# Performance work log

Measured on AMD Instinct MI355X. Metric: run time of the kernel, lower is better.

The kernel has to match this reference:

```python
import jax, jax.numpy as jnp
import numpy as np

N, C, H, K = 100000, 64, 8, 16
D = C // H  # head_dim = 8


def setup_inputs() -> dict:
    key = jax.random.key(0)
    ks = jax.random.split(key, 7)
    s = 1.0 / np.sqrt(C)
    return {
        "feats": jax.random.normal(ks[0], (N, C), jnp.float32),
        "knn_idx": jax.random.randint(ks[1], (N, K), 0, N, jnp.int32),
        "Wq": jax.random.normal(ks[2], (C, C), jnp.float32) * s,
        "Wk": jax.random.normal(ks[3], (C, C), jnp.float32) * s,
        "Wv": jax.random.normal(ks[4], (C, C), jnp.float32) * s,
        "Wo": jax.random.normal(ks[5], (C, C), jnp.float32) * s,
        "bo": jnp.zeros((C,), jnp.float32),
    }


def reference(feats, knn_idx, Wq, Wk, Wv, Wo, bo):
    # Projections (torch Linear y = x @ W^T expressed with pre-transposed W)
    q = (feats @ Wq).reshape(N, H, D)          # [N,H,D]
    k_feat = (feats @ Wk).reshape(N, H, D)     # [N,H,D]
    v = (feats @ Wv).reshape(N, H, D)          # [N,H,D]

    # Gather k-NN neighbors: [N,K,H,D]
    k_nb = k_feat[knn_idx]
    v_nb = v[knn_idx]

    # Scores: dot(q, k_neighbor) per head, scaled
    scores = jnp.einsum("nhd,nkhd->nkh", q, k_nb) / np.sqrt(D).astype(np.float32)
    attn = jax.nn.softmax(scores, axis=1)      # softmax over K neighbors

    out = jnp.einsum("nkh,nkhd->nhd", attn, v_nb).reshape(N, C)
    return out @ Wo + bo
```

## Files before the change

kernel.cpp:

```cpp
#include <hip/hip_runtime.h>
#include <hip/hip_fp16.h>
#include <math.h>

#define NPTS 100000
#define CDIM 64
#define KNN  16

typedef unsigned int uint;
typedef _Float16 f16x8 __attribute__((ext_vector_type(8)));
typedef float    f32x4 __attribute__((ext_vector_type(4)));

template <int CTRL>
__device__ __forceinline__ float dpp_add(float x) {
    int yi = __builtin_amdgcn_mov_dpp(__float_as_int(x), CTRL, 0xF, 0xF, true);
    return x + __int_as_float(yi);
}

__device__ __forceinline__ f16x8 load_bfrag(const float* W, int ks, int quad,
                                            int ct, int m) {
    const float* wp = W + (size_t)(ks * 32 + quad * 8) * 64 + ct * 16 + m;
    f16x8 b;
    #pragma unroll
    for (int j = 0; j < 8; ++j) b[j] = (_Float16)wp[j * 64];
    return b;
}

__device__ __forceinline__ f16x8 load_afrag(const float* fp, int ks, int quad) {
    const float4 x0 = *(const float4*)(fp + ks * 32 + quad * 8);
    const float4 x1 = *(const float4*)(fp + ks * 32 + quad * 8 + 4);
    f16x8 a;
    a[0] = (_Float16)x0.x; a[1] = (_Float16)x0.y;
    a[2] = (_Float16)x0.z; a[3] = (_Float16)x0.w;
    a[4] = (_Float16)x1.x; a[5] = (_Float16)x1.y;
    a[6] = (_Float16)x1.z; a[7] = (_Float16)x1.w;
    return a;
}

__global__ __launch_bounds__(256) void proj_qkv(
    const float* __restrict__ feats,
    const float* __restrict__ Wq, const float* __restrict__ Wk,
    const float* __restrict__ Wv,
    float* __restrict__ q, uint* __restrict__ kv)
{
    const int lane = threadIdx.x & 63;
    const int m = lane & 15, quad = lane >> 4;

    f16x8 Bf[3][4][2];
    #pragma unroll
    for (int ct = 0; ct < 4; ++ct)
        #pragma unroll
        for (int ks = 0; ks < 2; ++ks) {
            Bf[0][ct][ks] = load_bfrag(Wq, ks, quad, ct, m);
            Bf[1][ct][ks] = load_bfrag(Wk, ks, quad, ct, m);
            Bf[2][ct][ks] = load_bfrag(Wv, ks, quad, ct, m);
        }

    const int wid = blockIdx.x * 4 + (threadIdx.x >> 6);
    const int nw = gridDim.x * 4;
    for (int tile = wid; tile < NPTS / 16; tile += nw) {
        const int r0 = tile * 16;
        const float* fp = feats + (size_t)(r0 + m) * 64;
        f16x8 Af0 = load_afrag(fp, 0, quad);
        f16x8 Af1 = load_afrag(fp, 1, quad);

        #pragma unroll
        for (int ct = 0; ct < 4; ++ct) {
            f32x4 aq = {0.f, 0.f, 0.f, 0.f};
            f32x4 ak = {0.f, 0.f, 0.f, 0.f};
            f32x4 av = {0.f, 0.f, 0.f, 0.f};
            aq = __builtin_amdgcn_mfma_f32_16x16x32_f16(Af0, Bf[0][ct][0], aq, 0, 0, 0);
            aq = __builtin_amdgcn_mfma_f32_16x16x32_f16(Af1, Bf[0][ct][1], aq, 0, 0, 0);
            ak = __builtin_amdgcn_mfma_f32_16x16x32_f16(Af0, Bf[1][ct][0], ak, 0, 0, 0);
            ak = __builtin_amdgcn_mfma_f32_16x16x32_f16(Af1, Bf[1][ct][1], ak, 0, 0, 0);
            av = __builtin_amdgcn_mfma_f32_16x16x32_f16(Af0, Bf[2][ct][0], av, 0, 0, 0);
            av = __builtin_amdgcn_mfma_f32_16x16x32_f16(Af1, Bf[2][ct][1], av, 0, 0, 0);

            const int col = ct * 16 + m;
            #pragma unroll
            for (int r = 0; r < 4; ++r) {
                const size_t off = (size_t)(r0 + quad * 4 + r) * 64 + col;
                q[off] = aq[r];
                kv[off] = (uint)__half_as_ushort(__float2half(ak[r]))
                        | ((uint)__half_as_ushort(__float2half(av[r])) << 16);
            }
        }
    }
}

__global__ __launch_bounds__(256) void attn_mid(
    const float* __restrict__ q, const uint* __restrict__ kv,
    const int* __restrict__ knn, float* __restrict__ o_mid)
{
    const int t = threadIdx.x;
    const int lane = t & 63;
    const int n = blockIdx.x * 4 + (t >> 6);
    const int ns = __builtin_amdgcn_readfirstlane(n);

    const float qv = q[(size_t)n * 64 + lane];

    const int* kr = knn + (size_t)ns * KNN;
    int idx[KNN];
    #pragma unroll
    for (int i = 0; i < KNN; ++i) idx[i] = kr[i];

    float sc[KNN], vr[KNN];
    #pragma unroll
    for (int i = 0; i < KNN; ++i) {
        const uint w = kv[(size_t)idx[i] * 64 + lane];
        const float2 kvf = __half22float2(*(const __half2*)&w);
        vr[i] = kvf.y;
        float p = qv * kvf.x;
        p = dpp_add<0xB1>(p);
        p = dpp_add<0x4E>(p);
        p = dpp_add<0x141>(p);
        sc[i] = p * 0.3535533905932738f;
    }

    float m = sc[0];
    #pragma unroll
    for (int i = 1; i < KNN; ++i) m = fmaxf(m, sc[i]);
    float s = 0.f;
    #pragma unroll
    for (int i = 0; i < KNN; ++i) { sc[i] = __expf(sc[i] - m); s += sc[i]; }
    const float inv = 1.f / s;

    float acc = 0.f;
    #pragma unroll
    for (int i = 0; i < KNN; ++i) acc += sc[i] * vr[i];

    o_mid[(size_t)n * 64 + lane] = acc * inv;
}

__global__ __launch_bounds__(256) void out_proj(
    const float* __restrict__ o_mid, const float* __restrict__ Wo,
    const float* __restrict__ bo, float* __restrict__ out)
{
    const int lane = threadIdx.x & 63;
    const int m = lane & 15, quad = lane >> 4;

    f16x8 Bf[4][2];
    float bias[4];
    #pragma unroll
    for (int ct = 0; ct < 4; ++ct) {
        bias[ct] = bo[ct * 16 + m];
        #pragma unroll
        for (int ks = 0; ks < 2; ++ks)
            Bf[ct][ks] = load_bfrag(Wo, ks, quad, ct, m);
    }

    const int wid = blockIdx.x * 4 + (threadIdx.x >> 6);
    const int nw = gridDim.x * 4;
    for (int tile = wid; tile < NPTS / 16; tile += nw) {
        const int r0 = tile * 16;
        const float* fp = o_mid + (size_t)(r0 + m) * 64;
        f16x8 Af0 = load_afrag(fp, 0, quad);
        f16x8 Af1 = load_afrag(fp, 1, quad);

        #pragma unroll
        for (int ct = 0; ct < 4; ++ct) {
            f32x4 ac = {0.f, 0.f, 0.f, 0.f};
            ac = __builtin_amdgcn_mfma_f32_16x16x32_f16(Af0, Bf[ct][0], ac, 0, 0, 0);
            ac = __builtin_amdgcn_mfma_f32_16x16x32_f16(Af1, Bf[ct][1], ac, 0, 0, 0);

            const int col = ct * 16 + m;
            #pragma unroll
            for (int r = 0; r < 4; ++r)
                out[(size_t)(r0 + quad * 4 + r) * 64 + col] = ac[r] + bias[ct];
        }
    }
}

extern "C" void kernel_launch(void* const* d_in, const int* in_sizes, int n_in,
                              void* d_out, int out_size, void* d_ws, size_t ws_size,
                              hipStream_t stream) {
    const float* feats = (const float*)d_in[0];
    const int*   knn   = (const int*)d_in[1];
    const float* Wq    = (const float*)d_in[2];
    const float* Wk    = (const float*)d_in[3];
    const float* Wv    = (const float*)d_in[4];
    const float* Wo    = (const float*)d_in[5];
    const float* bo    = (const float*)d_in[6];
    float* out = (float*)d_out;

    float* q     = (float*)d_ws;
    uint*  kvbuf = (uint*)(q + (size_t)NPTS * CDIM);
    float* o_mid = (float*)(kvbuf + (size_t)NPTS * CDIM);

    proj_qkv<<<512, 256, 0, stream>>>(feats, Wq, Wk, Wv, q, kvbuf);
    attn_mid<<<NPTS / 4, 256, 0, stream>>>(q, kvbuf, knn, o_mid);
    out_proj<<<512, 256, 0, stream>>>(o_mid, Wo, bo, out);
}
```

Before: 169.3 us.

## Fuse attention with output projection, prepack weight fragments, store q in fp16

Adds a one-block kernel that packs all four weight matrices into fp16 MFMA fragment layout once, so the projection kernels load fragments with a single vector load instead of strided scalar gathers. The attention kernel now handles 16 points per block, stages the attention output in shared memory and applies the output projection with MFMA in place, which removes the o_mid round trip through global memory and one launch. q is stored as fp16, halving its traffic at a small precision cost, and proj_qkv switches to one tile per wave with many more blocks. This adds an extra tiny launch and a block barrier in the attention kernel.

```diff
diff --git a/kernel.cpp b/kernel.cpp
--- a/kernel.cpp
+++ b/kernel.cpp
@@ -16,13 +16,27 @@
     return x + __int_as_float(yi);
 }
 
-__device__ __forceinline__ f16x8 load_bfrag(const float* W, int ks, int quad,
-                                            int ct, int m) {
-    const float* wp = W + (size_t)(ks * 32 + quad * 8) * 64 + ct * 16 + m;
-    f16x8 b;
-    #pragma unroll
-    for (int j = 0; j < 8; ++j) b[j] = (_Float16)wp[j * 64];
-    return b;
+
+__global__ __launch_bounds__(256) void pack_w(
+    const float* __restrict__ Wq, const float* __restrict__ Wk,
+    const float* __restrict__ Wv, const float* __restrict__ Wo,
+    __half* __restrict__ frag)
+{
+    const float* Ws[4] = {Wq, Wk, Wv, Wo};
+    f16x8* fp = (f16x8*)frag;
+    for (int e = threadIdx.x; e < 2048; e += 256) {
+        const int lane = e & 63;
+        const int ks   = (e >> 6) & 1;
+        const int ct   = (e >> 7) & 3;
+        const int mat  = e >> 9;
+        const int m = lane & 15, quad = lane >> 4;
+        const float* W = Ws[mat];
+        f16x8 b;
+        #pragma unroll
+        for (int j = 0; j < 8; ++j)
+            b[j] = (_Float16)W[(size_t)(ks * 32 + quad * 8 + j) * 64 + ct * 16 + m];
+        fp[e] = b;
+    }
 }
 
 __device__ __forceinline__ f16x8 load_afrag(const float* fp, int ks, int quad) {
@@ -37,137 +51,136 @@
 }
 
 __global__ __launch_bounds__(256) void proj_qkv(
-    const float* __restrict__ feats,
-    const float* __restrict__ Wq, const float* __restrict__ Wk,
-    const float* __restrict__ Wv,
-    float* __restrict__ q, uint* __restrict__ kv)
+    const float* __restrict__ feats, const __half* __restrict__ frag,
+    __half* __restrict__ q, uint* __restrict__ kv)
 {
+    const int wid = blockIdx.x * 4 + (threadIdx.x >> 6);
+    if (wid >= NPTS / 16) return;
     const int lane = threadIdx.x & 63;
     const int m = lane & 15, quad = lane >> 4;
 
+    const f16x8* fp = (const f16x8*)frag;
     f16x8 Bf[3][4][2];
     #pragma unroll
-    for (int ct = 0; ct < 4; ++ct)
-        #pragma unroll
-        for (int ks = 0; ks < 2; ++ks) {
-            Bf[0][ct][ks] = load_bfrag(Wq, ks, quad, ct, m);
-            Bf[1][ct][ks] = load_bfrag(Wk, ks, quad, ct, m);
-            Bf[2][ct][ks] = load_bfrag(Wv, ks, quad, ct, m);
+    for (int mat = 0; mat < 3; ++mat)
+        #pragma unroll
+        for (int ct = 0; ct < 4; ++ct)
+            #pragma unroll
+            for (int ks = 0; ks < 2; ++ks)
+                Bf[mat][ct][ks] = fp[((mat * 4 + ct) * 2 + ks) * 64 + lane];
+
+    const int r0 = wid * 16;
+    const float* ap = feats + (size_t)(r0 + m) * 64;
+    const f16x8 Af0 = load_afrag(ap, 0, quad);
+    const f16x8 Af1 = load_afrag(ap, 1, quad);
+
+    #pragma unroll
+    for (int ct = 0; ct < 4; ++ct) {
+        f32x4 aq = {0.f, 0.f, 0.f, 0.f};
+        f32x4 ak = {0.f, 0.f, 0.f, 0.f};
+        f32x4 av = {0.f, 0.f, 0.f, 0.f};
+        aq = __builtin_amdgcn_mfma_f32_16x16x32_f16(Af0, Bf[0][ct][0], aq, 0, 0, 0);
+        aq = __builtin_amdgcn_mfma_f32_16x16x32_f16(Af1, Bf[0][ct][1], aq, 0, 0, 0);
+        ak = __builtin_amdgcn_mfma_f32_16x16x32_f16(Af0, Bf[1][ct][0], ak, 0, 0, 0);
+        ak = __builtin_amdgcn_mfma_f32_16x16x32_f16(Af1, Bf[1][ct][1], ak, 0, 0, 0);
+        av = __builtin_amdgcn_mfma_f32_16x16x32_f16(Af0, Bf[2][ct][0], av, 0, 0, 0);
+        av = __builtin_amdgcn_mfma_f32_16x16x32_f16(Af1, Bf[2][ct][1], av, 0, 0, 0);
+
+        const int col = ct * 16 + m;
+        #pragma unroll
+        for (int r = 0; r < 4; ++r) {
+            const size_t off = (size_t)(r0 + quad * 4 + r) * 64 + col;
+            q[off] = __float2half(aq[r]);
+            kv[off] = (uint)__half_as_ushort(__float2half(ak[r]))
+                    | ((uint)__half_as_ushort(__float2half(av[r])) << 16);
         }
-
-    const int wid = blockIdx.x * 4 + (threadIdx.x >> 6);
-    const int nw = gridDim.x * 4;
-    for (int tile = wid; tile < NPTS / 16; tile += nw) {
-        const int r0 = tile * 16;
-        const float* fp = feats + (size_t)(r0 + m) * 64;
-        f16x8 Af0 = load_afrag(fp, 0, quad);
-        f16x8 Af1 = load_afrag(fp, 1, quad);
-
-        #pragma unroll
-        for (int ct = 0; ct < 4; ++ct) {
-            f32x4 aq = {0.f, 0.f, 0.f, 0.f};
-            f32x4 ak = {0.f, 0.f, 0.f, 0.f};
-            f32x4 av = {0.f, 0.f, 0.f, 0.f};
-            aq = __builtin_amdgcn_mfma_f32_16x16x32_f16(Af0, Bf[0][ct][0], aq, 0, 0, 0);
-            aq = __builtin_amdgcn_mfma_f32_16x16x32_f16(Af1, Bf[0][ct][1], aq, 0, 0, 0);
-            ak = __builtin_amdgcn_mfma_f32_16x16x32_f16(Af0, Bf[1][ct][0], ak, 0, 0, 0);
-            ak = __builtin_amdgcn_mfma_f32_16x16x32_f16(Af1, Bf[1][ct][1], ak, 0, 0, 0);
-            av = __builtin_amdgcn_mfma_f32_16x16x32_f16(Af0, Bf[2][ct][0], av, 0, 0, 0);
-            av = __builtin_amdgcn_mfma_f32_16x16x32_f16(Af1, Bf[2][ct][1], av, 0, 0, 0);
-
-            const int col = ct * 16 + m;
-            #pragma unroll
-            for (int r = 0; r < 4; ++r) {
-                const size_t off = (size_t)(r0 + quad * 4 + r) * 64 + col;
-                q[off] = aq[r];
-                kv[off] = (uint)__half_as_ushort(__float2half(ak[r]))
-                        | ((uint)__half_as_ushort(__float2half(av[r])) << 16);
-            }
-        }
-    }
-}
-
-__global__ __launch_bounds__(256) void attn_mid(
-    const float* __restrict__ q, const uint* __restrict__ kv,
-    const int* __restrict__ knn, float* __restrict__ o_mid)
+    }
+}
+
+__global__ __launch_bounds__(256) void attn_out(
+    const __half* __restrict__ q, const uint* __restrict__ kv,
+    const int* __restrict__ knn, const __half* __restrict__ frag,
+    const float* __restrict__ bo, float* __restrict__ out)
 {
+    __shared__ float sO[16][68];
     const int t = threadIdx.x;
     const int lane = t & 63;
-    const int n = blockIdx.x * 4 + (t >> 6);
-    const int ns = __builtin_amdgcn_readfirstlane(n);
-
-    const float qv = q[(size_t)n * 64 + lane];
-
-    const int* kr = knn + (size_t)ns * KNN;
-    int idx[KNN];
+    const int w = t >> 6;
+    const int m = lane & 15, quad = lane >> 4;
+
+    const f16x8* fpb = (const f16x8*)frag;
+    const f16x8 Wf0 = fpb[((3 * 4 + w) * 2 + 0) * 64 + lane];
+    const f16x8 Wf1 = fpb[((3 * 4 + w) * 2 + 1) * 64 + lane];
+    const float bias = bo[w * 16 + m];
+
+    const int n0 = blockIdx.x * 16;
+
+    #pragma unroll 1
+    for (int p = 0; p < 4; ++p) {
+        const int n = n0 + w * 4 + p;
+        const int ns = __builtin_amdgcn_readfirstlane(n);
+
+        const float qv = __half2float(q[(size_t)n * 64 + lane]);
+
+        const int* kr = knn + (size_t)ns * KNN;
+        int idx[KNN];
+        #pragma unroll
+        for (int i = 0; i < KNN; ++i) idx[i] = kr[i];
+
+        float sc[KNN], vr[KNN];
+        #pragma unroll
+        for (int i = 0; i < KNN; ++i) {
+            const uint wv = kv[(size_t)idx[i] * 64 + lane];
+            const float2 kvf = __half22float2(*(const __half2*)&wv);
+            vr[i] = kvf.y;
+            float pr = qv * kvf.x;
+            pr = dpp_add<0xB1>(pr);
+            pr = dpp_add<0x4E>(pr);
+            pr = dpp_add<0x141>(pr);
+            sc[i] = pr * 0.3535533905932738f;
+        }
+
+        float mx = sc[0];
+        #pragma unroll
+        for (int i = 1; i < KNN; ++i) mx = fmaxf(mx, sc[i]);
+        float s = 0.f;
+        #pragma unroll
+        for (int i = 0; i < KNN; ++i) { sc[i] = __expf(sc[i] - mx); s += sc[i]; }
+        const float inv = 1.f / s;
+
+        float acc = 0.f;
+        #pragma unroll
+        for (int i = 0; i < KNN; ++i) acc += sc[i] * vr[i];
+
+        sO[w * 4 + p][lane] = acc * inv;
+    }
+    __syncthreads();
+
+    const float* ap = &sO[m][0];
+    f16x8 Af0, Af1;
+    {
+        const float4 x0 = *(const float4*)(ap + quad * 8);
+        const float4 x1 = *(const float4*)(ap + quad * 8 + 4);
+        Af0[0] = (_Float16)x0.x; Af0[1] = (_Float16)x0.y;
+        Af0[2] = (_Float16)x0.z; Af0[3] = (_Float16)x0.w;
+        Af0[4] = (_Float16)x1.x; Af0[5] = (_Float16)x1.y;
+        Af0[6] = (_Float16)x1.z; Af0[7] = (_Float16)x1.w;
+        const float4 y0 = *(const float4*)(ap + 32 + quad * 8);
+        const float4 y1 = *(const float4*)(ap + 32 + quad * 8 + 4);
+        Af1[0] = (_Float16)y0.x; Af1[1] = (_Float16)y0.y;
+        Af1[2] = (_Float16)y0.z; Af1[3] = (_Float16)y0.w;
+        Af1[4] = (_Float16)y1.x; Af1[5] = (_Float16)y1.y;
+        Af1[6] = (_Float16)y1.z; Af1[7] = (_Float16)y1.w;
+    }
+
+    f32x4 ac = {0.f, 0.f, 0.f, 0.f};
+    ac = __builtin_amdgcn_mfma_f32_16x16x32_f16(Af0, Wf0, ac, 0, 0, 0);
+    ac = __builtin_amdgcn_mfma_f32_16x16x32_f16(Af1, Wf1, ac, 0, 0, 0);
+
+    const int col = w * 16 + m;
     #pragma unroll
-    for (int i = 0; i < KNN; ++i) idx[i] = kr[i];
-
-    float sc[KNN], vr[KNN];
-    #pragma unroll
-    for (int i = 0; i < KNN; ++i) {
-        const uint w = kv[(size_t)idx[i] * 64 + lane];
-        const float2 kvf = __half22float2(*(const __half2*)&w);
-        vr[i] = kvf.y;
-        float p = qv * kvf.x;
-        p = dpp_add<0xB1>(p);
-        p = dpp_add<0x4E>(p);
-        p = dpp_add<0x141>(p);
-        sc[i] = p * 0.3535533905932738f;
-    }
-
-    float m = sc[0];
-    #pragma unroll
-    for (int i = 1; i < KNN; ++i) m = fmaxf(m, sc[i]);
-    float s = 0.f;
-    #pragma unroll
-    for (int i = 0; i < KNN; ++i) { sc[i] = __expf(sc[i] - m); s += sc[i]; }
-    const float inv = 1.f / s;
-
-    float acc = 0.f;
-    #pragma unroll
-    for (int i = 0; i < KNN; ++i) acc += sc[i] * vr[i];
-
-    o_mid[(size_t)n * 64 + lane] = acc * inv;
-}
-
-__global__ __launch_bounds__(256) void out_proj(
-    const float* __restrict__ o_mid, const float* __restrict__ Wo,
-    const float* __restrict__ bo, float* __restrict__ out)
-{
-    const int lane = threadIdx.x & 63;
-    const int m = lane & 15, quad = lane >> 4;
-
-    f16x8 Bf[4][2];
-    float bias[4];
-    #pragma unroll
-    for (int ct = 0; ct < 4; ++ct) {
-        bias[ct] = bo[ct * 16 + m];
-        #pragma unroll
-        for (int ks = 0; ks < 2; ++ks)
-            Bf[ct][ks] = load_bfrag(Wo, ks, quad, ct, m);
-    }
-
-    const int wid = blockIdx.x * 4 + (threadIdx.x >> 6);
-    const int nw = gridDim.x * 4;
-    for (int tile = wid; tile < NPTS / 16; tile += nw) {
-        const int r0 = tile * 16;
-        const float* fp = o_mid + (size_t)(r0 + m) * 64;
-        f16x8 Af0 = load_afrag(fp, 0, quad);
-        f16x8 Af1 = load_afrag(fp, 1, quad);
-
-        #pragma unroll
-        for (int ct = 0; ct < 4; ++ct) {
-            f32x4 ac = {0.f, 0.f, 0.f, 0.f};
-            ac = __builtin_amdgcn_mfma_f32_16x16x32_f16(Af0, Bf[ct][0], ac, 0, 0, 0);
-            ac = __builtin_amdgcn_mfma_f32_16x16x32_f16(Af1, Bf[ct][1], ac, 0, 0, 0);
-
-            const int col = ct * 16 + m;
-            #pragma unroll
-            for (int r = 0; r < 4; ++r)
-                out[(size_t)(r0 + quad * 4 + r) * 64 + col] = ac[r] + bias[ct];
-        }
-    }
+    for (int r = 0; r < 4; ++r)
+        out[(size_t)(n0 + quad * 4 + r) * 64 + col] = ac[r] + bias;
 }
 
 extern "C" void kernel_launch(void* const* d_in, const int* in_sizes, int n_in,
@@ -182,11 +195,12 @@
     const float* bo    = (const float*)d_in[6];
     float* out = (float*)d_out;
 
-    float* q     = (float*)d_ws;
-    uint*  kvbuf = (uint*)(q + (size_t)NPTS * CDIM);
-    float* o_mid = (float*)(kvbuf + (size_t)NPTS * CDIM);
-
-    proj_qkv<<<512, 256, 0, stream>>>(feats, Wq, Wk, Wv, q, kvbuf);
-    attn_mid<<<NPTS / 4, 256, 0, stream>>>(q, kvbuf, knn, o_mid);
-    out_proj<<<512, 256, 0, stream>>>(o_mid, Wo, bo, out);
-}
+    __half* frag = (__half*)d_ws;
+    __half* q_h  = (__half*)((char*)d_ws + 32768);
+    uint*   kvb  = (uint*)((char*)d_ws + 32768 +
+                           (size_t)NPTS * CDIM * sizeof(__half));
+
+    pack_w<<<1, 256, 0, stream>>>(Wq, Wk, Wv, Wo, frag);
+    proj_qkv<<<(NPTS / 16 + 3) / 4, 256, 0, stream>>>(feats, frag, q_h, kvb);
+    attn_out<<<NPTS / 16, 256, 0, stream>>>(q_h, kvb, knn, frag, bo, out);
+}
```

New measurement: 158.2 us. 1.07x faster.
